# Kernel tuning notes

Hardware: AMD Instinct MI355X
Metric: run time of the kernel (lower is better)

## Reference

```python
import jax, jax.numpy as jnp
import numpy as np
import math

BLOCK = 8
N_COEFF = BLOCK * BLOCK  # 64
N_SAMPLE = 250
SEED = 0  # args.seed

# zigzag order: flat index m*8+n from the hardcoded loc table
ZIGZAG = jnp.array([
    0, 1, 8, 16, 9, 2, 3, 10, 17, 24, 32, 25, 18, 11, 4, 5,
    12, 19, 26, 33, 40, 48, 41, 34, 27, 20, 13, 6, 7, 14, 21, 28,
    35, 42, 49, 56, 57, 50, 43, 36, 29, 22, 15, 23, 30, 37, 44, 51,
    58, 59, 52, 45, 38, 31, 39, 46, 53, 60, 61, 54, 47, 55, 62, 63
], dtype=jnp.int32)


def dct_matrix():
    Q = np.zeros((BLOCK, BLOCK), dtype=np.float32)
    Q[0, :] = math.sqrt(1.0 / BLOCK)
    for i in range(1, BLOCK):
        for j in range(BLOCK):
            Q[i, j] = math.sqrt(2.0 / BLOCK) * math.cos((2 * j + 1) * math.pi * i / (2.0 * BLOCK))
    return jnp.asarray(Q)


def setup_inputs() -> dict:
    key = jax.random.key(0)
    x = jax.random.uniform(key, (64, 3, 512, 512), dtype=jnp.float32)
    return {"x": x}


def reference(x):
    Q = dct_matrix()
    # rgb -> ycbcr, luminance channel only (module discards Cb/Cr)
    x255 = x * 255.0
    y = (0.299 * x255[:, 0] + 0.587 * x255[:, 1] + 0.114 * x255[:, 2]) / 255.0  # [B,H,W]
    B, H, W = y.shape
    a, b = H // BLOCK, W // BLOCK
    # split into 8x8 blocks: [B, a, b, 8, 8]
    blocks = y.reshape(B, a, BLOCK, b, BLOCK).transpose(0, 1, 3, 2, 4)
    # per-block 2D DCT: Q @ block @ Q^T, batched as one einsum
    dct = jnp.einsum('ij,nabjk,lk->nabil', Q, blocks, Q)  # [B,a,b,8,8]
    image_dct_result = dct.transpose(0, 1, 3, 2, 4).reshape(B, 1, H, W)
    # zigzag gather over flattened block coefficients -> [B, 64, a*b]
    dist = dct.reshape(B, a * b, N_COEFF)[:, :, ZIGZAG].transpose(0, 2, 1)
    # per (sample, coefficient) random permutation sampling of 250 blocks
    keys = jax.random.split(jax.random.key(SEED), B * N_COEFF)
    idx = jax.vmap(lambda k: jax.random.permutation(k, a * b)[:N_SAMPLE])(keys)
    idx = idx.reshape(B, N_COEFF, N_SAMPLE)
    dct_coeff_sample = jnp.take_along_axis(dist, idx, axis=2)  # [B,64,250]
    return image_dct_result, dct_coeff_sample
```

## Files before the change

kernel.cpp:

```cpp
#include <hip/hip_runtime.h>
#include <hip/hip_bf16.h>
#include <cstdint>


#define BATCH 64
#define HW 512
#define NBLK 4096
#define NSAMPLE 250
#define IMG_ELEMS (HW * HW)

#define A0 0.35355339059327373f
#define A1 0.49039264020161522f
#define A2 0.46193976625564337f
#define A3 0.41573480615127262f
#define A4 0.35355339059327379f
#define A5 0.27778511650980111f
#define A6 0.19134171618254492f
#define A7 0.09754516100806412f

__constant__ float Qc[8][8] = {
    { A0,  A0,  A0,  A0,  A0,  A0,  A0,  A0},
    { A1,  A3,  A5,  A7, -A7, -A5, -A3, -A1},
    { A2,  A6, -A6, -A2, -A2, -A6,  A6,  A2},
    { A3, -A7, -A1, -A5,  A5,  A1,  A7, -A3},
    { A4, -A4, -A4,  A4,  A4, -A4, -A4,  A4},
    { A5, -A1,  A7,  A3, -A3, -A7,  A1, -A5},
    { A6, -A2,  A2, -A6, -A6,  A2, -A2,  A6},
    { A7, -A5,  A3, -A1,  A1, -A3,  A5, -A7},
};

__constant__ int ZIGZAG[64] = {
    0, 1, 8, 16, 9, 2, 3, 10, 17, 24, 32, 25, 18, 11, 4, 5,
    12, 19, 26, 33, 40, 48, 41, 34, 27, 20, 13, 6, 7, 14, 21, 28,
    35, 42, 49, 56, 57, 50, 43, 36, 29, 22, 15, 23, 30, 37, 44, 51,
    58, 59, 52, 45, 38, 31, 39, 46, 53, 60, 61, 54, 47, 55, 62, 63
};

__global__ __launch_bounds__(256) void dct_kernel(const float* __restrict__ x,
                                                  float* __restrict__ out) {
    int g = blockIdx.x * 256 + threadIdx.x;
    int b  = g >> 12;
    int rr = g & 4095;
    int ai = rr >> 6, bi = rr & 63;
    int row0 = ai * 8, col0 = bi * 8;
    size_t ib = (size_t)b * 3 * IMG_ELEMS;

    float acc[8][8];
#pragma unroll
    for (int k = 0; k < 8; ++k) {
        size_t off = ib + (size_t)(row0 + k) * HW + col0;
        float4 r0 = *(const float4*)(x + off);
        float4 r1 = *(const float4*)(x + off + 4);
        float4 g0 = *(const float4*)(x + off + IMG_ELEMS);
        float4 g1 = *(const float4*)(x + off + IMG_ELEMS + 4);
        float4 b0 = *(const float4*)(x + off + 2 * IMG_ELEMS);
        float4 b1 = *(const float4*)(x + off + 2 * IMG_ELEMS + 4);
        float R[8] = {r0.x, r0.y, r0.z, r0.w, r1.x, r1.y, r1.z, r1.w};
        float G[8] = {g0.x, g0.y, g0.z, g0.w, g1.x, g1.y, g1.z, g1.w};
        float B[8] = {b0.x, b0.y, b0.z, b0.w, b1.x, b1.y, b1.z, b1.w};
        float y[8];
#pragma unroll
        for (int j = 0; j < 8; ++j)
            y[j] = (0.299f * (R[j] * 255.0f) + 0.587f * (G[j] * 255.0f) +
                    0.114f * (B[j] * 255.0f)) / 255.0f;
#pragma unroll
        for (int i = 0; i < 8; ++i) {
            float q = Qc[i][k];
#pragma unroll
            for (int j = 0; j < 8; ++j)
                acc[i][j] = (k == 0) ? q * y[j] : acc[i][j] + q * y[j];
        }
    }

    size_t ob = (size_t)b * IMG_ELEMS;
#pragma unroll
    for (int i = 0; i < 8; ++i) {
        float d[8];
#pragma unroll
        for (int j = 0; j < 8; ++j) {
            float s = 0.0f;
#pragma unroll
            for (int k = 0; k < 8; ++k) s += acc[i][k] * Qc[j][k];
            d[j] = s;
        }
        float4* o = (float4*)(out + ob + (size_t)(row0 + i) * HW + col0);
        o[0] = make_float4(d[0], d[1], d[2], d[3]);
        o[1] = make_float4(d[4], d[5], d[6], d[7]);
    }
}

__device__ __forceinline__ uint32_t rotl32(uint32_t v, int d) {
    return (v << d) | (v >> (32 - d));
}

__device__ __forceinline__ void tf2x32(uint32_t k0, uint32_t k1,
                                       uint32_t x0, uint32_t x1,
                                       uint32_t& o0, uint32_t& o1) {
    uint32_t ks0 = k0, ks1 = k1, ks2 = k0 ^ k1 ^ 0x1BD11BDAu;
    x0 += ks0; x1 += ks1;
#define TF_R(r) { x0 += x1; x1 = rotl32(x1, r); x1 ^= x0; }
    TF_R(13) TF_R(15) TF_R(26) TF_R(6)
    x0 += ks1; x1 += ks2 + 1u;
    TF_R(17) TF_R(29) TF_R(16) TF_R(24)
    x0 += ks2; x1 += ks0 + 2u;
    TF_R(13) TF_R(15) TF_R(26) TF_R(6)
    x0 += ks0; x1 += ks1 + 3u;
    TF_R(17) TF_R(29) TF_R(16) TF_R(24)
    x0 += ks1; x1 += ks2 + 4u;
    TF_R(13) TF_R(15) TF_R(26) TF_R(6)
    x0 += ks2; x1 += ks0 + 5u;
#undef TF_R
    o0 = x0; o1 = x1;
}

__device__ __forceinline__ void rank4096(
    uint32_t s0, uint32_t s1,
    uint64_t* __restrict__ pack, uint32_t* __restrict__ hist32,
    uint32_t* __restrict__ slot32, bool zero_slot,
    int tid, int w, int lane, uint32_t* __restrict__ wsum,
    uint32_t keys[8], uint32_t ranks[8]) {
    uint16_t* hist16 = (uint16_t*)hist32;

    __syncthreads();
#pragma unroll
    for (int q = 0; q < 4; ++q) hist32[tid + q * 512] = 0u;
    if (zero_slot) {
#pragma unroll
        for (int q = 0; q < 4; ++q) slot32[tid + q * 512] = 0xFFFFFFFFu;
    }
#pragma unroll
    for (int e = 0; e < 8; ++e) {
        uint32_t o0, o1;
        tf2x32(s0, s1, 0u, (uint32_t)(tid + e * 512), o0, o1);
        keys[e] = o0 ^ o1;
    }
    __syncthreads();

#pragma unroll
    for (int e = 0; e < 8; ++e) {
        uint32_t b = keys[e] >> 20;
        atomicAdd(&hist32[b >> 1], 1u << ((b & 1) << 4));
    }
    __syncthreads();

    uint4 wv = ((const uint4*)hist32)[tid];
    uint32_t c0 = wv.x & 0xFFFFu, c1 = wv.x >> 16;
    uint32_t c2 = wv.y & 0xFFFFu, c3 = wv.y >> 16;
    uint32_t c4 = wv.z & 0xFFFFu, c5 = wv.z >> 16;
    uint32_t c6 = wv.w & 0xFFFFu, c7 = wv.w >> 16;
    uint32_t ssum = c0 + c1 + c2 + c3 + c4 + c5 + c6 + c7;
    uint32_t sc = ssum;
#pragma unroll
    for (int off = 1; off < 64; off <<= 1) {
        uint32_t t = __shfl_up(sc, off);
        if (lane >= off) sc += t;
    }
    if (lane == 63) wsum[w] = sc;
    __syncthreads();
    uint32_t ex = sc - ssum;
    for (int ww = 0; ww < w; ++ww) ex += wsum[ww];
    uint32_t p0 = ex, p1 = p0 + c0, p2 = p1 + c1, p3 = p2 + c2;
    uint32_t p4 = p3 + c3, p5 = p4 + c4, p6 = p5 + c5, p7 = p6 + c6;
    uint4 ov;
    ov.x = p0 | (p1 << 16); ov.y = p2 | (p3 << 16);
    ov.z = p4 | (p5 << 16); ov.w = p6 | (p7 << 16);
    ((uint4*)hist32)[tid] = ov;
    __syncthreads();

#pragma unroll
    for (int e = 0; e < 8; ++e) {
        uint32_t b = keys[e] >> 20;
        uint32_t sh = (b & 1) << 4;
        uint32_t old = atomicAdd(&hist32[b >> 1], 1u << sh);
        uint32_t pos = (old >> sh) & 0xFFFFu;
        pack[pos] = ((uint64_t)keys[e] << 32) | (uint32_t)(tid + e * 512);
    }
    __syncthreads();

#pragma unroll
    for (int e = 0; e < 8; ++e) {
        uint32_t b = keys[e] >> 20;
        uint32_t start = b ? (uint32_t)hist16[b - 1] : 0u;
        uint32_t end = (uint32_t)hist16[b];
        uint64_t self = ((uint64_t)keys[e] << 32) | (uint32_t)(tid + e * 512);
        uint32_t r = start;
        for (uint32_t p = start; p < end; ++p)
            r += (pack[p] < self) ? 1u : 0u;
        ranks[e] = r;
    }
}

__global__ __launch_bounds__(512) void sample_kernel(const float* __restrict__ img,
                                                     float* __restrict__ out2) {
    __shared__ __align__(16) uint64_t pack[NBLK];
    __shared__ __align__(16) uint32_t hist32[2048];
    __shared__ __align__(16) uint32_t slot32[2048];
    __shared__ uint32_t wsum[8];
    uint16_t* slot16 = (uint16_t*)slot32;

    const int tid = threadIdx.x;
    const int w = tid >> 6;
    const int lane = tid & 63;
    const int gb = blockIdx.x;

    uint32_t k0, k1, n0, n1, sA0, sA1, sB0, sB1;
    tf2x32(0u, 0u, 0u, (uint32_t)gb, k0, k1);
    tf2x32(k0, k1, 0u, 0u, n0, n1);
    tf2x32(k0, k1, 0u, 1u, sA0, sA1);
    tf2x32(n0, n1, 0u, 1u, sB0, sB1);

    uint32_t keys[8], ranks[8];

    rank4096(sB0, sB1, pack, hist32, slot32, true, tid, w, lane, wsum, keys, ranks);
#pragma unroll
    for (int e = 0; e < 8; ++e)
        if (ranks[e] < NSAMPLE) slot16[tid + e * 512] = (uint16_t)ranks[e];

    rank4096(sA0, sA1, pack, hist32, slot32, false, tid, w, lane, wsum, keys, ranks);

    int b = gb >> 6, c = gb & 63;
    int z = ZIGZAG[c];
    int i0z = z >> 3, j0z = z & 7;
    const float* base = img + (size_t)b * IMG_ELEMS;
#pragma unroll
    for (int e = 0; e < 8; ++e) {
        uint32_t s = slot16[ranks[e]];
        if (s != 0xFFFFu) {
            int i = tid + e * 512;
            int ai = i >> 6, bi = i & 63;
            out2[(size_t)gb * NSAMPLE + s] =
                base[(size_t)(ai * 8 + i0z) * HW + (bi * 8 + j0z)];
        }
    }
}

extern "C" void kernel_launch(void* const* d_in, const int* in_sizes, int n_in,
                              void* d_out, int out_size, void* d_ws, size_t ws_size,
                              hipStream_t stream) {
    const float* x = (const float*)d_in[0];
    float* out = (float*)d_out;
    dct_kernel<<<(BATCH * NBLK) / 256, 256, 0, stream>>>(x, out);
    sample_kernel<<<BATCH * 64, 512, 0, stream>>>(out, out + (size_t)BATCH * IMG_ELEMS);
}
```

Measured before the change: 421.9 us.

## Cooperative LDS-staged DCT and 32-bit packed keys in sampling rank

The DCT kernel now has each workgroup handle one 8-row strip of half the image width. Threads load rows cooperatively, stage luminance in LDS, and each thread computes one output row of one block, which cuts per-thread register pressure and makes global accesses more coalesced. In the sampling kernel, the rank step records each key's position within its bucket from the histogram atomic, so the second atomic pass goes away. Keys are packed into 32 bits (the low 20 key bits plus the index) instead of 64 bits, which halves LDS traffic for the comparisons. The 32-bit packing relies on the bucket already fixing the top 12 key bits, so ordering within a bucket is unchanged.

```diff
diff --git a/kernel.cpp b/kernel.cpp
--- a/kernel.cpp
+++ b/kernel.cpp
@@ -38,17 +38,21 @@
 
 __global__ __launch_bounds__(256) void dct_kernel(const float* __restrict__ x,
                                                   float* __restrict__ out) {
-    int g = blockIdx.x * 256 + threadIdx.x;
-    int b  = g >> 12;
-    int rr = g & 4095;
-    int ai = rr >> 6, bi = rr & 63;
-    int row0 = ai * 8, col0 = bi * 8;
-    size_t ib = (size_t)b * 3 * IMG_ELEMS;
-
-    float acc[8][8];
-#pragma unroll
-    for (int k = 0; k < 8; ++k) {
-        size_t off = ib + (size_t)(row0 + k) * HW + col0;
+    __shared__ float ylds[8 * 8 * 32];
+
+    const int t = threadIdx.x;
+    const int wg = blockIdx.x;
+    const int b = wg >> 7;
+    const int ai = (wg >> 1) & 63;
+    const int h = wg & 1;
+    const int row0 = ai * 8;
+    const int colbase = h * 256;
+
+    {
+        const int k = t >> 5;
+        const int cg = t & 31;
+        size_t off = (size_t)b * 3 * IMG_ELEMS + (size_t)(row0 + k) * HW +
+                     colbase + cg * 8;
         float4 r0 = *(const float4*)(x + off);
         float4 r1 = *(const float4*)(x + off + 4);
         float4 g0 = *(const float4*)(x + off + IMG_ELEMS);
@@ -58,35 +62,43 @@
         float R[8] = {r0.x, r0.y, r0.z, r0.w, r1.x, r1.y, r1.z, r1.w};
         float G[8] = {g0.x, g0.y, g0.z, g0.w, g1.x, g1.y, g1.z, g1.w};
         float B[8] = {b0.x, b0.y, b0.z, b0.w, b1.x, b1.y, b1.z, b1.w};
-        float y[8];
+#pragma unroll
+        for (int jj = 0; jj < 8; ++jj) {
+            float y = (0.299f * (R[jj] * 255.0f) + 0.587f * (G[jj] * 255.0f) +
+                       0.114f * (B[jj] * 255.0f)) / 255.0f;
+            ylds[k * 256 + jj * 32 + cg] = y;
+        }
+    }
+    __syncthreads();
+
+    const int i = t >> 5;
+    const int bi = t & 31;
+    float qrow[8];
+#pragma unroll
+    for (int k = 0; k < 8; ++k) qrow[k] = Qc[i][k];
+
+    float acc[8];
+#pragma unroll
+    for (int j = 0; j < 8; ++j) acc[j] = 0.0f;
+#pragma unroll
+    for (int k = 0; k < 8; ++k) {
 #pragma unroll
         for (int j = 0; j < 8; ++j)
-            y[j] = (0.299f * (R[j] * 255.0f) + 0.587f * (G[j] * 255.0f) +
-                    0.114f * (B[j] * 255.0f)) / 255.0f;
-#pragma unroll
-        for (int i = 0; i < 8; ++i) {
-            float q = Qc[i][k];
-#pragma unroll
-            for (int j = 0; j < 8; ++j)
-                acc[i][j] = (k == 0) ? q * y[j] : acc[i][j] + q * y[j];
-        }
-    }
-
-    size_t ob = (size_t)b * IMG_ELEMS;
-#pragma unroll
-    for (int i = 0; i < 8; ++i) {
-        float d[8];
-#pragma unroll
-        for (int j = 0; j < 8; ++j) {
-            float s = 0.0f;
-#pragma unroll
-            for (int k = 0; k < 8; ++k) s += acc[i][k] * Qc[j][k];
-            d[j] = s;
-        }
-        float4* o = (float4*)(out + ob + (size_t)(row0 + i) * HW + col0);
-        o[0] = make_float4(d[0], d[1], d[2], d[3]);
-        o[1] = make_float4(d[4], d[5], d[6], d[7]);
-    }
+            acc[j] += qrow[k] * ylds[k * 256 + j * 32 + bi];
+    }
+
+    float d[8];
+#pragma unroll
+    for (int j = 0; j < 8; ++j) {
+        float s = 0.0f;
+#pragma unroll
+        for (int k = 0; k < 8; ++k) s += acc[k] * Qc[j][k];
+        d[j] = s;
+    }
+    float4* o = (float4*)(out + (size_t)b * IMG_ELEMS +
+                          (size_t)(row0 + i) * HW + colbase + bi * 8);
+    o[0] = make_float4(d[0], d[1], d[2], d[3]);
+    o[1] = make_float4(d[4], d[5], d[6], d[7]);
 }
 
 __device__ __forceinline__ uint32_t rotl32(uint32_t v, int d) {
@@ -115,10 +127,10 @@
 
 __device__ __forceinline__ void rank4096(
     uint32_t s0, uint32_t s1,
-    uint64_t* __restrict__ pack, uint32_t* __restrict__ hist32,
+    uint32_t* __restrict__ pack32, uint32_t* __restrict__ hist32,
     uint32_t* __restrict__ slot32, bool zero_slot,
     int tid, int w, int lane, uint32_t* __restrict__ wsum,
-    uint32_t keys[8], uint32_t ranks[8]) {
+    uint32_t ranks[8]) {
     uint16_t* hist16 = (uint16_t*)hist32;
 
     __syncthreads();
@@ -128,6 +140,7 @@
 #pragma unroll
         for (int q = 0; q < 4; ++q) slot32[tid + q * 512] = 0xFFFFFFFFu;
     }
+    uint32_t keys[8];
 #pragma unroll
     for (int e = 0; e < 8; ++e) {
         uint32_t o0, o1;
@@ -136,10 +149,13 @@
     }
     __syncthreads();
 
-#pragma unroll
-    for (int e = 0; e < 8; ++e) {
-        uint32_t b = keys[e] >> 20;
-        atomicAdd(&hist32[b >> 1], 1u << ((b & 1) << 4));
+    uint32_t ord[8];
+#pragma unroll
+    for (int e = 0; e < 8; ++e) {
+        uint32_t bkt = keys[e] >> 20;
+        uint32_t sh = (bkt & 1) << 4;
+        uint32_t old = atomicAdd(&hist32[bkt >> 1], 1u << sh);
+        ord[e] = (old >> sh) & 0xFFFFu;
     }
     __syncthreads();
 
@@ -159,40 +175,40 @@
     __syncthreads();
     uint32_t ex = sc - ssum;
     for (int ww = 0; ww < w; ++ww) ex += wsum[ww];
-    uint32_t p0 = ex, p1 = p0 + c0, p2 = p1 + c1, p3 = p2 + c2;
-    uint32_t p4 = p3 + c3, p5 = p4 + c4, p6 = p5 + c5, p7 = p6 + c6;
+    uint32_t p1 = ex + c0, p2 = p1 + c1, p3 = p2 + c2, p4 = p3 + c3;
+    uint32_t p5 = p4 + c4, p6 = p5 + c5, p7 = p6 + c6, p8 = p7 + c7;
     uint4 ov;
-    ov.x = p0 | (p1 << 16); ov.y = p2 | (p3 << 16);
-    ov.z = p4 | (p5 << 16); ov.w = p6 | (p7 << 16);
+    ov.x = p1 | (p2 << 16); ov.y = p3 | (p4 << 16);
+    ov.z = p5 | (p6 << 16); ov.w = p7 | (p8 << 16);
     ((uint4*)hist32)[tid] = ov;
     __syncthreads();
 
 #pragma unroll
     for (int e = 0; e < 8; ++e) {
-        uint32_t b = keys[e] >> 20;
-        uint32_t sh = (b & 1) << 4;
-        uint32_t old = atomicAdd(&hist32[b >> 1], 1u << sh);
-        uint32_t pos = (old >> sh) & 0xFFFFu;
-        pack[pos] = ((uint64_t)keys[e] << 32) | (uint32_t)(tid + e * 512);
-    }
-    __syncthreads();
-
-#pragma unroll
-    for (int e = 0; e < 8; ++e) {
-        uint32_t b = keys[e] >> 20;
-        uint32_t start = b ? (uint32_t)hist16[b - 1] : 0u;
-        uint32_t end = (uint32_t)hist16[b];
-        uint64_t self = ((uint64_t)keys[e] << 32) | (uint32_t)(tid + e * 512);
+        uint32_t bkt = keys[e] >> 20;
+        uint32_t start = bkt ? (uint32_t)hist16[bkt - 1] : 0u;
+        pack32[start + ord[e]] =
+            ((keys[e] & 0xFFFFFu) << 12) | (uint32_t)(tid + e * 512);
+        ord[e] = start;
+    }
+    __syncthreads();
+
+#pragma unroll
+    for (int e = 0; e < 8; ++e) {
+        uint32_t bkt = keys[e] >> 20;
+        uint32_t start = ord[e];
+        uint32_t end = (uint32_t)hist16[bkt];
+        uint32_t self = ((keys[e] & 0xFFFFFu) << 12) | (uint32_t)(tid + e * 512);
         uint32_t r = start;
         for (uint32_t p = start; p < end; ++p)
-            r += (pack[p] < self) ? 1u : 0u;
+            r += (pack32[p] < self) ? 1u : 0u;
         ranks[e] = r;
     }
 }
 
 __global__ __launch_bounds__(512) void sample_kernel(const float* __restrict__ img,
                                                      float* __restrict__ out2) {
-    __shared__ __align__(16) uint64_t pack[NBLK];
+    __shared__ __align__(16) uint32_t pack32[NBLK];
     __shared__ __align__(16) uint32_t hist32[2048];
     __shared__ __align__(16) uint32_t slot32[2048];
     __shared__ uint32_t wsum[8];
@@ -209,14 +225,14 @@
     tf2x32(k0, k1, 0u, 1u, sA0, sA1);
     tf2x32(n0, n1, 0u, 1u, sB0, sB1);
 
-    uint32_t keys[8], ranks[8];
-
-    rank4096(sB0, sB1, pack, hist32, slot32, true, tid, w, lane, wsum, keys, ranks);
+    uint32_t ranks[8];
+
+    rank4096(sB0, sB1, pack32, hist32, slot32, true, tid, w, lane, wsum, ranks);
 #pragma unroll
     for (int e = 0; e < 8; ++e)
         if (ranks[e] < NSAMPLE) slot16[tid + e * 512] = (uint16_t)ranks[e];
 
-    rank4096(sA0, sA1, pack, hist32, slot32, false, tid, w, lane, wsum, keys, ranks);
+    rank4096(sA0, sA1, pack32, hist32, slot32, false, tid, w, lane, wsum, ranks);
 
     int b = gb >> 6, c = gb & 63;
     int z = ZIGZAG[c];
@@ -239,6 +255,6 @@
                               hipStream_t stream) {
     const float* x = (const float*)d_in[0];
     float* out = (float*)d_out;
-    dct_kernel<<<(BATCH * NBLK) / 256, 256, 0, stream>>>(x, out);
+    dct_kernel<<<BATCH * 128, 256, 0, stream>>>(x, out);
     sample_kernel<<<BATCH * 64, 512, 0, stream>>>(out, out + (size_t)BATCH * IMG_ELEMS);
 }
```

New measurement: 414.4 us. About the same (-1.8%).
